# Kernel tuning notes

Hardware: AMD Instinct MI355X
Metric: run time of the kernel (lower is better)

Reference implementation:

```python
import jax, jax.numpy as jnp
import numpy as np


def ste_sign(x):
    # Forward: q(x) = +1 if x >= 0 else -1.
    # Backward: clipped straight-through estimator (identity on |x| <= 1).
    clipped = jnp.clip(x, -1.0, 1.0)
    binary = jnp.where(x >= 0, 1.0, -1.0).astype(x.dtype)
    return clipped + jax.lax.stop_gradient(binary - clipped)


BATCH = 16384
IN_FEATURES = 4096
UNITS = 512


def setup_inputs() -> dict:
    key = jax.random.key(0)
    kx, kw = jax.random.split(key)
    x = jax.random.normal(kx, (BATCH, IN_FEATURES), dtype=jnp.float32)
    # Latent full-precision kernel (kept in [-1,1]-ish range like a constrained BNN kernel)
    W = jax.random.normal(kw, (IN_FEATURES, UNITS), dtype=jnp.float32) * 0.5
    b = jnp.zeros((UNITS,), dtype=jnp.float32)
    return {"x": x, "W": W, "b": b}


def reference(x, W, b):
    # QuantizedDense: binarize inputs and kernel to +/-1, then standard dense matmul.
    xq = ste_sign(x)                # [B, F]
    Wq = ste_sign(W)                # [F, U]
    return jnp.dot(xq, Wq) + b      # [B, U]
```

## Files before the change

### kernel.cpp

```cpp
#include <hip/hip_runtime.h>
#include <stdint.h>


#define BATCH  16384
#define UNITS  512
#define KDIM   4096
#define KSTEP  64
#define NSTEP  (KDIM / KSTEP)
#define NPER   (NSTEP / 4)
#define MROWS  32

typedef int v4i  __attribute__((ext_vector_type(4)));
typedef int v16i __attribute__((ext_vector_type(16)));

__global__ __launch_bounds__(256) void pack_w_kernel(const float* __restrict__ W,
                                                     uint8_t* __restrict__ Wb2) {
    int t  = blockIdx.x * 256 + threadIdx.x;
    int n  = t & 511;
    int k0 = (t >> 9) * 8;
    unsigned long long m = 0;
    #pragma unroll
    for (int j = 0; j < 8; ++j) {
        float v = W[(size_t)(k0 + j) * UNITS + n];
        m |= ((v < 0.f) ? 0xFFull : 0x01ull) << (8 * j);
    }
    int s  = k0 >> 6;
    int kk = k0 & 63;
    int ks = kk >> 5;
    int hi = (kk & 31) >> 4;
    int lane = (n & 31) + 32 * hi;
    size_t a = ((((size_t)s * 16 + (n >> 5)) * 2 + ks) * 64 + lane) * 16 + (kk & 15);
    *reinterpret_cast<unsigned long long*>(Wb2 + a) = m;
}

__device__ __forceinline__ uint32_t sgn4(float4 v) {
    uint32_t b0 = v.x < 0.f ? 0xFFu : 0x01u;
    uint32_t b1 = v.y < 0.f ? 0xFFu : 0x01u;
    uint32_t b2 = v.z < 0.f ? 0xFFu : 0x01u;
    uint32_t b3 = v.w < 0.f ? 0xFFu : 0x01u;
    return b0 | (b1 << 8) | (b2 << 16) | (b3 << 24);
}

#define STEP(PB, SIP, Q)                                                       \
    {                                                                          \
        const uint8_t* _b = bbase + (size_t)(4 * (Q) + (SIP)) * 32768;         \
        v4i b0 = *reinterpret_cast<const v4i*>(_b);                            \
        v4i b1 = *reinterpret_cast<const v4i*>(_b + 1024);                     \
        v4i af0 = *reinterpret_cast<const v4i*>(                               \
            &Af[(PB) * 8192 + ((SIP) * 2) * 1024 + l * 16]);                   \
        v4i af1 = *reinterpret_cast<const v4i*>(                               \
            &Af[(PB) * 8192 + ((SIP) * 2 + 1) * 1024 + l * 16]);               \
        __builtin_amdgcn_s_setprio(1);                                         \
        acc = __builtin_amdgcn_mfma_i32_32x32x32_i8(af0, b0, acc, 0, 0, 0);    \
        acc = __builtin_amdgcn_mfma_i32_32x32x32_i8(af1, b1, acc, 0, 0, 0);    \
        __builtin_amdgcn_s_setprio(0);                                         \
    }

#define PERIOD(Q, PB)                                                          \
    {                                                                          \
        STEP(PB, 0, Q);                                                        \
        const int _sc0 = (4 * (Q) + 4 + sp0 < NSTEP) ? 4 * (Q) + 4 + sp0 : NSTEP - 1; \
        float4 xq0 = *reinterpret_cast<const float4*>(xp0 + (size_t)_sc0 * KSTEP);    \
        STEP(PB, 1, Q);                                                        \
        const int _sc1 = (4 * (Q) + 4 + sp1 < NSTEP) ? 4 * (Q) + 4 + sp1 : NSTEP - 1; \
        float4 xq1 = *reinterpret_cast<const float4*>(xp0 + (size_t)_sc1 * KSTEP);    \
        STEP(PB, 2, Q);                                                        \
        STEP(PB, 3, Q);                                                        \
        *reinterpret_cast<uint32_t*>(&Af[((PB) ^ 1) * 8192 + aw0]) = sgn4(xq0);\
        *reinterpret_cast<uint32_t*>(&Af[((PB) ^ 1) * 8192 + aw1]) = sgn4(xq1);\
        __syncthreads();                                                       \
    }

__global__ __launch_bounds__(1024, 2) void mm_kernel(const float* __restrict__ x,
                                                     const uint8_t* __restrict__ Wb2,
                                                     const float* __restrict__ bias,
                                                     float* __restrict__ C) {
    __shared__ __attribute__((aligned(16))) uint8_t Af[2 * 8 * 1024];
    const int t   = threadIdx.x;
    const int l   = t & 63;
    const int wv  = t >> 6;
    const int lr  = l & 31;
    const int hi  = l >> 5;
    const int row0 = blockIdx.x * MROWS;

    const int sp0 = t >> 9;
    const int sp1 = (t + 1024) >> 9;
    const int fa0 = t & 511;
    const int ar0 = fa0 >> 4, ak0 = (fa0 & 15) * 4;
    const int aw0 = (sp0 * 2 + (ak0 >> 5)) * 1024
                  + ((ar0 & 31) + 32 * ((ak0 >> 4) & 1)) * 16 + (ak0 & 15);
    const int aw1 = (sp1 * 2 + (ak0 >> 5)) * 1024
                  + ((ar0 & 31) + 32 * ((ak0 >> 4) & 1)) * 16 + (ak0 & 15);
    const float* xp0 = x + (size_t)(row0 + ar0) * KDIM + ak0;
    const uint8_t* bbase = Wb2 + wv * 2048 + (size_t)l * 16;

    v16i acc;
    #pragma unroll
    for (int e = 0; e < 16; ++e) acc[e] = 0;

    {
        float4 xq0 = *reinterpret_cast<const float4*>(xp0 + (size_t)sp0 * KSTEP);
        float4 xq1 = *reinterpret_cast<const float4*>(xp0 + (size_t)sp1 * KSTEP);
        *reinterpret_cast<uint32_t*>(&Af[aw0]) = sgn4(xq0);
        *reinterpret_cast<uint32_t*>(&Af[aw1]) = sgn4(xq1);
        __syncthreads();
    }

    #pragma unroll 1
    for (int q = 0; q < NPER; q += 2) {
        PERIOD(q,     0);
        PERIOD(q + 1, 1);
    }

    {
        const int col = wv * 32 + lr;
        const float bv = bias[col];
        #pragma unroll
        for (int r = 0; r < 16; ++r) {
            int row = row0 + (r & 3) + 8 * (r >> 2) + 4 * hi;
            C[(size_t)row * UNITS + col] = (float)acc[r] + bv;
        }
    }
}

extern "C" void kernel_launch(void* const* d_in, const int* in_sizes, int n_in,
                              void* d_out, int out_size, void* d_ws, size_t ws_size,
                              hipStream_t stream) {
    const float* x = (const float*)d_in[0];
    const float* W = (const float*)d_in[1];
    const float* b = (const float*)d_in[2];
    float* out = (float*)d_out;

    uint8_t* Wb2 = (uint8_t*)d_ws;

    pack_w_kernel<<<(512 * 512) / 256, 256, 0, stream>>>(W, Wb2);
    mm_kernel<<<BATCH / MROWS, 1024, 0, stream>>>(x, Wb2, b, out);
}
```

Before: 104.6 us.

## Retile matmul to 64x256 blocks with two accumulators per wave

```diff
diff --git a/kernel.cpp b/kernel.cpp
--- a/kernel.cpp
+++ b/kernel.cpp
@@ -8,7 +8,8 @@
 #define KSTEP  64
 #define NSTEP  (KDIM / KSTEP)
 #define NPER   (NSTEP / 4)
-#define MROWS  32
+#define MROWS  64
+#define NCOLS  256
 
 typedef int v4i  __attribute__((ext_vector_type(4)));
 typedef int v16i __attribute__((ext_vector_type(16)));
@@ -41,68 +42,86 @@
     return b0 | (b1 << 8) | (b2 << 16) | (b3 << 24);
 }
 
+
 #define STEP(PB, SIP, Q)                                                       \
     {                                                                          \
         const uint8_t* _b = bbase + (size_t)(4 * (Q) + (SIP)) * 32768;         \
         v4i b0 = *reinterpret_cast<const v4i*>(_b);                            \
         v4i b1 = *reinterpret_cast<const v4i*>(_b + 1024);                     \
-        v4i af0 = *reinterpret_cast<const v4i*>(                               \
-            &Af[(PB) * 8192 + ((SIP) * 2) * 1024 + l * 16]);                   \
-        v4i af1 = *reinterpret_cast<const v4i*>(                               \
-            &Af[(PB) * 8192 + ((SIP) * 2 + 1) * 1024 + l * 16]);               \
+        const uint8_t* _a = &Af[(PB) * 16384 + (SIP) * 4096 + l * 16];         \
+        v4i a00 = *reinterpret_cast<const v4i*>(_a);                           \
+        v4i a01 = *reinterpret_cast<const v4i*>(_a + 1024);                    \
+        v4i a10 = *reinterpret_cast<const v4i*>(_a + 2048);                    \
+        v4i a11 = *reinterpret_cast<const v4i*>(_a + 3072);                    \
         __builtin_amdgcn_s_setprio(1);                                         \
-        acc = __builtin_amdgcn_mfma_i32_32x32x32_i8(af0, b0, acc, 0, 0, 0);    \
-        acc = __builtin_amdgcn_mfma_i32_32x32x32_i8(af1, b1, acc, 0, 0, 0);    \
+        acc0 = __builtin_amdgcn_mfma_i32_32x32x32_i8(a00, b0, acc0, 0, 0, 0);  \
+        acc0 = __builtin_amdgcn_mfma_i32_32x32x32_i8(a01, b1, acc0, 0, 0, 0);  \
+        acc1 = __builtin_amdgcn_mfma_i32_32x32x32_i8(a10, b0, acc1, 0, 0, 0);  \
+        acc1 = __builtin_amdgcn_mfma_i32_32x32x32_i8(a11, b1, acc1, 0, 0, 0);  \
         __builtin_amdgcn_s_setprio(0);                                         \
+    }
+
+#define XLD2(XA, XB, S)                                                        \
+    {                                                                          \
+        const int _sc = ((S) < NSTEP) ? (S) : NSTEP - 1;                       \
+        XA = *reinterpret_cast<const float4*>(xr0 + (size_t)_sc * KSTEP);      \
+        XB = *reinterpret_cast<const float4*>(xr0 + (size_t)32 * KDIM          \
+                                                  + (size_t)_sc * KSTEP);      \
+    }
+
+#define XCM2(PB, SIP, XA, XB)                                                  \
+    {                                                                          \
+        *reinterpret_cast<uint32_t*>(                                          \
+            &Af[(PB) * 16384 + (SIP) * 4096 + awk]) = sgn4(XA);                \
+        *reinterpret_cast<uint32_t*>(                                          \
+            &Af[(PB) * 16384 + (SIP) * 4096 + 2048 + awk]) = sgn4(XB);         \
     }
 
 #define PERIOD(Q, PB)                                                          \
     {                                                                          \
-        STEP(PB, 0, Q);                                                        \
-        const int _sc0 = (4 * (Q) + 4 + sp0 < NSTEP) ? 4 * (Q) + 4 + sp0 : NSTEP - 1; \
-        float4 xq0 = *reinterpret_cast<const float4*>(xp0 + (size_t)_sc0 * KSTEP);    \
-        STEP(PB, 1, Q);                                                        \
-        const int _sc1 = (4 * (Q) + 4 + sp1 < NSTEP) ? 4 * (Q) + 4 + sp1 : NSTEP - 1; \
-        float4 xq1 = *reinterpret_cast<const float4*>(xp0 + (size_t)_sc1 * KSTEP);    \
-        STEP(PB, 2, Q);                                                        \
-        STEP(PB, 3, Q);                                                        \
-        *reinterpret_cast<uint32_t*>(&Af[((PB) ^ 1) * 8192 + aw0]) = sgn4(xq0);\
-        *reinterpret_cast<uint32_t*>(&Af[((PB) ^ 1) * 8192 + aw1]) = sgn4(xq1);\
+        float4 xa0, xb0, xa1, xb1, xa2, xb2, xa3, xb3;                         \
+        STEP(PB, 0, Q); XLD2(xa0, xb0, 4 * (Q) + 4);                           \
+        STEP(PB, 1, Q); XLD2(xa1, xb1, 4 * (Q) + 5);                           \
+        STEP(PB, 2, Q); XLD2(xa2, xb2, 4 * (Q) + 6);                           \
+        STEP(PB, 3, Q); XLD2(xa3, xb3, 4 * (Q) + 7);                           \
+        XCM2((PB) ^ 1, 0, xa0, xb0);                                           \
+        XCM2((PB) ^ 1, 1, xa1, xb1);                                           \
+        XCM2((PB) ^ 1, 2, xa2, xb2);                                           \
+        XCM2((PB) ^ 1, 3, xa3, xb3);                                           \
         __syncthreads();                                                       \
     }
 
-__global__ __launch_bounds__(1024, 2) void mm_kernel(const float* __restrict__ x,
-                                                     const uint8_t* __restrict__ Wb2,
-                                                     const float* __restrict__ bias,
-                                                     float* __restrict__ C) {
-    __shared__ __attribute__((aligned(16))) uint8_t Af[2 * 8 * 1024];
+__global__ __launch_bounds__(512, 1) void mm_kernel(const float* __restrict__ x,
+                                                    const uint8_t* __restrict__ Wb2,
+                                                    const float* __restrict__ bias,
+                                                    float* __restrict__ C) {
+    __shared__ __attribute__((aligned(16))) uint8_t Af[2 * 16384];
     const int t   = threadIdx.x;
     const int l   = t & 63;
     const int wv  = t >> 6;
     const int lr  = l & 31;
     const int hi  = l >> 5;
-    const int row0 = blockIdx.x * MROWS;
+    const int bx  = blockIdx.x;
+    const int row0 = (bx >> 1) * MROWS;
+    const int cb8  = (bx & 1) * 8;
 
-    const int sp0 = t >> 9;
-    const int sp1 = (t + 1024) >> 9;
-    const int fa0 = t & 511;
-    const int ar0 = fa0 >> 4, ak0 = (fa0 & 15) * 4;
-    const int aw0 = (sp0 * 2 + (ak0 >> 5)) * 1024
-                  + ((ar0 & 31) + 32 * ((ak0 >> 4) & 1)) * 16 + (ak0 & 15);
-    const int aw1 = (sp1 * 2 + (ak0 >> 5)) * 1024
-                  + ((ar0 & 31) + 32 * ((ak0 >> 4) & 1)) * 16 + (ak0 & 15);
-    const float* xp0 = x + (size_t)(row0 + ar0) * KDIM + ak0;
-    const uint8_t* bbase = Wb2 + wv * 2048 + (size_t)l * 16;
+    const int trow = t >> 4;
+    const int tak  = (t & 15) * 4;
+    const int awk = (tak >> 5) * 1024
+                  + (trow + 32 * ((tak >> 4) & 1)) * 16 + (tak & 15);
+    const float* xr0 = x + (size_t)(row0 + trow) * KDIM + tak;
+    const uint8_t* bbase = Wb2 + (size_t)(cb8 + wv) * 2048 + (size_t)l * 16;
 
-    v16i acc;
+    v16i acc0, acc1;
     #pragma unroll
-    for (int e = 0; e < 16; ++e) acc[e] = 0;
+    for (int e = 0; e < 16; ++e) { acc0[e] = 0; acc1[e] = 0; }
 
     {
-        float4 xq0 = *reinterpret_cast<const float4*>(xp0 + (size_t)sp0 * KSTEP);
-        float4 xq1 = *reinterpret_cast<const float4*>(xp0 + (size_t)sp1 * KSTEP);
-        *reinterpret_cast<uint32_t*>(&Af[aw0]) = sgn4(xq0);
-        *reinterpret_cast<uint32_t*>(&Af[aw1]) = sgn4(xq1);
+        float4 xa, xb;
+        XLD2(xa, xb, 0); XCM2(0, 0, xa, xb);
+        XLD2(xa, xb, 1); XCM2(0, 1, xa, xb);
+        XLD2(xa, xb, 2); XCM2(0, 2, xa, xb);
+        XLD2(xa, xb, 3); XCM2(0, 3, xa, xb);
         __syncthreads();
     }
 
@@ -113,12 +132,13 @@
     }
 
     {
-        const int col = wv * 32 + lr;
+        const int col = cb8 * 32 + wv * 32 + lr;
         const float bv = bias[col];
         #pragma unroll
         for (int r = 0; r < 16; ++r) {
-            int row = row0 + (r & 3) + 8 * (r >> 2) + 4 * hi;
-            C[(size_t)row * UNITS + col] = (float)acc[r] + bv;
+            int crow = (r & 3) + 8 * (r >> 2) + 4 * hi;
+            C[(size_t)(row0 + crow) * UNITS + col]      = (float)acc0[r] + bv;
+            C[(size_t)(row0 + 32 + crow) * UNITS + col] = (float)acc1[r] + bv;
         }
     }
 }
@@ -134,5 +154,6 @@
     uint8_t* Wb2 = (uint8_t*)d_ws;
 
     pack_w_kernel<<<(512 * 512) / 256, 256, 0, stream>>>(W, Wb2);
-    mm_kernel<<<BATCH / MROWS, 1024, 0, stream>>>(x, Wb2, b, out);
+    mm_kernel<<<(BATCH / MROWS) * (UNITS / NCOLS), 512, 0, stream>>>(
+        x, Wb2, b, out);
 }
```

Result: slower. 128.7 us (+23.0%).
